# Kernel optimization log

Measured on AMD Instinct MI355X. Metric: run time of the kernel, lower is better.

The kernel has to match this reference:

```python
import jax, jax.numpy as jnp
import numpy as np

N = 100000      # nodes
E = 1600000     # edges (avg degree 16)
EL = 200000     # supervision (label) edges
D_IN, D_HID, D_OUT = 128, 128, 64


def setup_inputs() -> dict:
    key = jax.random.key(0)
    k = jax.random.split(key, 6)
    x = jax.random.normal(k[0], (N, D_IN), jnp.float32)
    edge_index = jax.random.randint(k[1], (2, E), 0, N, dtype=jnp.int32)
    edge_label_index = jax.random.randint(k[2], (2, EL), 0, N, dtype=jnp.int32)
    W1 = jax.random.normal(k[3], (D_IN, D_HID), jnp.float32) * (1.0 / np.sqrt(D_IN))
    b1 = jnp.zeros((D_HID,), jnp.float32)
    W2 = jax.random.normal(k[4], (D_HID, D_OUT), jnp.float32) * (1.0 / np.sqrt(D_HID))
    b2 = jnp.zeros((D_OUT,), jnp.float32)
    return {"x": x, "edge_index": edge_index, "edge_label_index": edge_label_index,
            "W1": W1, "b1": b1, "W2": W2, "b2": b2}


def gcn_layer(x, src, dst, W, b, n):
    """PyG-style GCNConv: linear -> sym-normalized scatter-add with self loops -> +bias."""
    h = x @ W                                   # [N, F]
    ones = jnp.ones(src.shape[0], h.dtype)
    deg = jax.ops.segment_sum(ones, dst, num_segments=n) + 1.0   # in-degree + self loop
    dinv = jax.lax.rsqrt(deg)                   # deg^{-1/2}
    norm = dinv[src] * dinv[dst]                # per-edge norm
    agg = jax.ops.segment_sum(h[src] * norm[:, None], dst, num_segments=n)
    agg = agg + h * (1.0 / deg)[:, None]        # self-loop contribution: dinv[i]^2
    return agg + b


def reference(x, edge_index, edge_label_index, W1, b1, W2, b2):
    src, dst = edge_index[0], edge_index[1]
    z = gcn_layer(x, src, dst, W1, b1, N)
    z = jax.nn.relu(z)                          # dropout omitted (eval mode)
    z = gcn_layer(z, src, dst, W2, b2, N)
    # decode: gather-dot over supervision edges
    return (z[edge_label_index[0]] * z[edge_label_index[1]]).sum(axis=-1)
```

## Files before the change

### kernel.cpp

```cpp
#include <hip/hip_runtime.h>
#include <stdint.h>

typedef __bf16 bf16x8 __attribute__((ext_vector_type(8)));
typedef float  floatx4 __attribute__((ext_vector_type(4)));
typedef __fp16 h2 __attribute__((ext_vector_type(2)));

__device__ __forceinline__ unsigned short f2b(float x){
    unsigned u = __float_as_uint(x);
    u = u + 0x7FFFu + ((u >> 16) & 1u);
    return (unsigned short)(u >> 16);
}
__device__ __forceinline__ float b2f(unsigned short h){
    return __uint_as_float(((unsigned)h) << 16);
}


__global__ __launch_bounds__(256) void k_scatter2(const int* __restrict__ src,
                                                  const int* __restrict__ dst,
                                                  int* __restrict__ gcur,
                                                  unsigned* __restrict__ slab,
                                                  int E_, int nbins){
    __shared__ int h[1024];
    int t = threadIdx.x, blk = blockIdx.x;
    for (int i = t; i < nbins; i += 256) h[i] = 0;
    __syncthreads();
    int base = blk * 8192;
    #pragma unroll
    for (int j = 0; j < 8; j++){
        int e = base + (j * 256 + t) * 4;
        if (e < E_){
            int4 d = *(const int4*)(dst + e);
            atomicAdd(&h[d.x >> 7], 1);
            atomicAdd(&h[d.y >> 7], 1);
            atomicAdd(&h[d.z >> 7], 1);
            atomicAdd(&h[d.w >> 7], 1);
        }
    }
    __syncthreads();
    for (int i = t; i < nbins; i += 256){
        int hv = h[i];
        h[i] = hv ? atomicAdd(&gcur[i], hv) : 0;
    }
    __syncthreads();
    #pragma unroll
    for (int j = 0; j < 8; j++){
        int e = base + (j * 256 + t) * 4;
        if (e < E_){
            int4 d = *(const int4*)(dst + e);
            int4 s = *(const int4*)(src + e);
            int p0 = atomicAdd(&h[d.x >> 7], 1);
            slab[(size_t)(d.x >> 7) * 4096 + p0] = ((unsigned)(d.x & 127) << 25) | (unsigned)s.x;
            int p1 = atomicAdd(&h[d.y >> 7], 1);
            slab[(size_t)(d.y >> 7) * 4096 + p1] = ((unsigned)(d.y & 127) << 25) | (unsigned)s.y;
            int p2 = atomicAdd(&h[d.z >> 7], 1);
            slab[(size_t)(d.z >> 7) * 4096 + p2] = ((unsigned)(d.z & 127) << 25) | (unsigned)s.z;
            int p3 = atomicAdd(&h[d.w >> 7], 1);
            slab[(size_t)(d.w >> 7) * 4096 + p3] = ((unsigned)(d.w & 127) << 25) | (unsigned)s.w;
        }
    }
}

__global__ __launch_bounds__(1024) void k_binscanB(const int* __restrict__ btot,
                                                   int* __restrict__ boff, int nbins){
    __shared__ int s[1024];
    int t = threadIdx.x;
    s[t] = (t < nbins) ? btot[t] : 0;
    __syncthreads();
    for (int o = 1; o < 1024; o <<= 1){
        int v = (t >= o) ? s[t - o] : 0;
        __syncthreads();
        s[t] += v;
        __syncthreads();
    }
    if (t == 0) boff[0] = 0;
    if (t < nbins) boff[t + 1] = s[t];
}

__global__ __launch_bounds__(256) void k_binsort(const unsigned* __restrict__ slab,
                                                 const int* __restrict__ boff,
                                                 int* __restrict__ csr,
                                                 int* __restrict__ cnt,
                                                 int* __restrict__ off,
                                                 float* __restrict__ dinv,
                                                 int n, int nbins){
    int b = blockIdx.x, t = threadIdx.x;
    int s0 = boff[b], len = boff[b + 1] - s0;
    if (len > 4096) len = 4096;
    const unsigned* seg = slab + (size_t)b * 4096;
    __shared__ int cl[128], sc[128], cur[128];
    __shared__ unsigned buf[4096], outb[4096];
    if (t < 128){ cl[t] = 0; cur[t] = 0; }
    __syncthreads();
    for (int i = t; i < len; i += 256) buf[i] = seg[i];
    __syncthreads();
    for (int i = t; i < len; i += 256) atomicAdd(&cl[buf[i] >> 25], 1);
    __syncthreads();
    if (t < 128) sc[t] = cl[t];
    __syncthreads();
    for (int o = 1; o < 128; o <<= 1){
        int v = 0;
        if (t < 128 && t >= o) v = sc[t - o];
        __syncthreads();
        if (t < 128) sc[t] += v;
        __syncthreads();
    }
    for (int i = t; i < len; i += 256){
        unsigned w = buf[i];
        int nd = (int)(w >> 25);
        int p = (sc[nd] - cl[nd]) + atomicAdd(&cur[nd], 1);
        outb[p] = w & 0x1FFFFFFu;
    }
    __syncthreads();
    for (int i = t; i < len; i += 256) csr[s0 + i] = (int)outb[i];
    if (t < 128){
        int node = b * 128 + t;
        if (node < n){
            cnt[node] = cl[t];
            off[node] = s0 + (sc[t] - cl[t]);
            dinv[node] = rsqrtf((float)cl[t] + 1.0f);
        }
    }
}

__global__ __launch_bounds__(256) void k_wconv(const float* __restrict__ W1,
                                               const float* __restrict__ W2,
                                               unsigned short* __restrict__ wf1,
                                               unsigned* __restrict__ w2p){
    int f = blockIdx.x * 256 + threadIdx.x;
    if (f < 2048){
        int lane = f & 63;
        int ctkc = f >> 6;
        int kc = ctkc & 3, ct = ctkc >> 2;
        int col = ct * 16 + (lane & 15);
        int k0  = kc * 32 + (lane >> 4) * 8;
        unsigned short* d = wf1 + (size_t)f * 8;
        #pragma unroll
        for (int j = 0; j < 8; j++) d[j] = f2b(W1[(k0 + j) * 128 + col]);
    } else if (f < 2048 + 4096){
        int lf = f - 2048;
        int kp = lf >> 6, lane = lf & 63;
        h2 p = __builtin_amdgcn_cvt_pkrtz(W2[(2 * kp) * 64 + lane],
                                          W2[(2 * kp + 1) * 64 + lane]);
        w2p[lf] = __builtin_bit_cast(unsigned, p);
    }
}

__global__ __launch_bounds__(256) void k_gemm1(const float* __restrict__ x,
                                               const unsigned short* __restrict__ wf,
                                               const float* __restrict__ dinv,
                                               unsigned short* __restrict__ hs, int n){
    __shared__ unsigned short Wl[16384];
    __shared__ unsigned short Al[64 * 136];
    int t = threadIdx.x;
    long rowBase = (long)blockIdx.x * 64;
    {
        const uint4* s4 = (const uint4*)wf;
        uint4* d4 = (uint4*)Wl;
        #pragma unroll
        for (int i = 0; i < 8; i++) d4[t + i * 256] = s4[t + i * 256];
    }
    {
        const float4* xs = (const float4*)(x + rowBase * 128);
        #pragma unroll
        for (int k = 0; k < 8; k++){
            int i = t + k * 256;
            int r = i >> 5, c4 = (i & 31) << 2;
            float4 v = make_float4(0.f, 0.f, 0.f, 0.f);
            if (rowBase + r < n) v = xs[i];
            unsigned lo = (unsigned)f2b(v.x) | ((unsigned)f2b(v.y) << 16);
            unsigned hi = (unsigned)f2b(v.z) | ((unsigned)f2b(v.w) << 16);
            *(uint2*)&Al[r * 136 + c4] = make_uint2(lo, hi);
        }
    }
    __syncthreads();
    int w = t >> 6, lane = t & 63, lr = lane & 15, q = lane >> 4;
    floatx4 zero = {0.f, 0.f, 0.f, 0.f};
    floatx4 acc[8];
    #pragma unroll
    for (int ct = 0; ct < 8; ct++) acc[ct] = zero;
    #pragma unroll
    for (int kc = 0; kc < 4; kc++){
        bf16x8 af = *(const bf16x8*)&Al[(w * 16 + lr) * 136 + kc * 32 + q * 8];
        #pragma unroll
        for (int ct = 0; ct < 8; ct++){
            bf16x8 bf = *(const bf16x8*)&Wl[((ct * 4 + kc) * 64 + lane) * 8];
            acc[ct] = __builtin_amdgcn_mfma_f32_16x16x32_bf16(af, bf, acc[ct], 0, 0, 0);
        }
    }
    long r0 = rowBase + w * 16 + q * 4;
    #pragma unroll
    for (int r = 0; r < 4; r++){
        long row = r0 + r;
        if (row >= n) continue;
        float dv = dinv[row];
        unsigned short* orow = hs + row * 128 + lr;
        #pragma unroll
        for (int ct = 0; ct < 8; ct++) orow[ct * 16] = f2b(acc[ct][r] * dv);
    }
}

__global__ __launch_bounds__(256) void k_agg1g2(const unsigned short* __restrict__ hs,
                                                const int* __restrict__ off,
                                                const int* __restrict__ cnt,
                                                const int* __restrict__ csr,
                                                const float* __restrict__ dinv,
                                                const float* __restrict__ b1,
                                                const unsigned* __restrict__ w2p,
                                                unsigned short* __restrict__ hs2,
                                                int n, int nwaves){
    __shared__ unsigned W2l[4096];
    __shared__ unsigned zp[4][64];
    int t = threadIdx.x;
    {
        const uint4* w4 = (const uint4*)w2p;
        uint4* d4 = (uint4*)W2l;
        #pragma unroll
        for (int i = 0; i < 4; i++) d4[t + i * 256] = w4[t + i * 256];
    }
    __syncthreads();
    int wband = t >> 6, lane = t & 63;
    float2 bb = ((const float2*)b1)[lane];
    for (int wid = blockIdx.x * 4 + wband; wid < n; wid += nwaves){
        size_t i = (size_t)wid;
        int start = off[wid], c = cnt[wid];
        unsigned v0 = *(const unsigned*)(hs + i * 128 + lane * 2);
        float a0 = b2f((unsigned short)v0);
        float a1 = b2f((unsigned short)(v0 >> 16));
        int j = 0;
        for (; j + 8 <= c; j += 8){
            size_t s0 = (size_t)csr[start + j + 0];
            size_t s1 = (size_t)csr[start + j + 1];
            size_t s2 = (size_t)csr[start + j + 2];
            size_t s3 = (size_t)csr[start + j + 3];
            size_t s4 = (size_t)csr[start + j + 4];
            size_t s5 = (size_t)csr[start + j + 5];
            size_t s6 = (size_t)csr[start + j + 6];
            size_t s7 = (size_t)csr[start + j + 7];
            unsigned w0 = *(const unsigned*)(hs + s0 * 128 + lane * 2);
            unsigned w1 = *(const unsigned*)(hs + s1 * 128 + lane * 2);
            unsigned w2 = *(const unsigned*)(hs + s2 * 128 + lane * 2);
            unsigned w3 = *(const unsigned*)(hs + s3 * 128 + lane * 2);
            unsigned w4 = *(const unsigned*)(hs + s4 * 128 + lane * 2);
            unsigned w5 = *(const unsigned*)(hs + s5 * 128 + lane * 2);
            unsigned w6 = *(const unsigned*)(hs + s6 * 128 + lane * 2);
            unsigned w7 = *(const unsigned*)(hs + s7 * 128 + lane * 2);
            a0 += b2f((unsigned short)w0); a1 += b2f((unsigned short)(w0 >> 16));
            a0 += b2f((unsigned short)w1); a1 += b2f((unsigned short)(w1 >> 16));
            a0 += b2f((unsigned short)w2); a1 += b2f((unsigned short)(w2 >> 16));
            a0 += b2f((unsigned short)w3); a1 += b2f((unsigned short)(w3 >> 16));
            a0 += b2f((unsigned short)w4); a1 += b2f((unsigned short)(w4 >> 16));
            a0 += b2f((unsigned short)w5); a1 += b2f((unsigned short)(w5 >> 16));
            a0 += b2f((unsigned short)w6); a1 += b2f((unsigned short)(w6 >> 16));
            a0 += b2f((unsigned short)w7); a1 += b2f((unsigned short)(w7 >> 16));
        }
        for (; j < c; j++){
            size_t s = (size_t)csr[start + j];
            unsigned v = *(const unsigned*)(hs + s * 128 + lane * 2);
            a0 += b2f((unsigned short)v);
            a1 += b2f((unsigned short)(v >> 16));
        }
        float dv = dinv[wid];
        float z0 = fmaxf(fmaf(dv, a0, bb.x), 0.f);
        float z1 = fmaxf(fmaf(dv, a1, bb.y), 0.f);
        zp[wband][lane] = __builtin_bit_cast(unsigned, __builtin_amdgcn_cvt_pkrtz(z0, z1));
        float acc0 = 0.f, acc1 = 0.f;
        #pragma unroll 8
        for (int kp = 0; kp < 64; kp += 2){
            h2 wa = __builtin_bit_cast(h2, W2l[kp * 64 + lane]);
            h2 wb = __builtin_bit_cast(h2, W2l[(kp + 1) * 64 + lane]);
            h2 za = __builtin_bit_cast(h2, zp[wband][kp]);
            h2 zb = __builtin_bit_cast(h2, zp[wband][kp + 1]);
            acc0 = __builtin_amdgcn_fdot2(za, wa, acc0, false);
            acc1 = __builtin_amdgcn_fdot2(zb, wb, acc1, false);
        }
        hs2[i * 64 + lane] = f2b((acc0 + acc1) * dv);
    }
}

__global__ __launch_bounds__(256) void k_agg2(const unsigned short* __restrict__ hs,
                                              const int* __restrict__ off,
                                              const int* __restrict__ cnt,
                                              const int* __restrict__ csr,
                                              const float* __restrict__ dinv,
                                              const float* __restrict__ b,
                                              unsigned short* __restrict__ z, int n){
    int wv = (blockIdx.x * 256 + threadIdx.x) >> 6;
    int lane = threadIdx.x & 63;
    int half = lane >> 5, hl = lane & 31;
    int node = wv * 2 + half;
    if (node >= n) return;
    size_t i = (size_t)node;
    int start = off[node], c = cnt[node];
    unsigned v0 = *(const unsigned*)(hs + i * 64 + hl * 2);
    float a0 = b2f((unsigned short)v0);
    float a1 = b2f((unsigned short)(v0 >> 16));
    int j = 0;
    for (; j + 8 <= c; j += 8){
        size_t s0 = (size_t)csr[start + j + 0];
        size_t s1 = (size_t)csr[start + j + 1];
        size_t s2 = (size_t)csr[start + j + 2];
        size_t s3 = (size_t)csr[start + j + 3];
        size_t s4 = (size_t)csr[start + j + 4];
        size_t s5 = (size_t)csr[start + j + 5];
        size_t s6 = (size_t)csr[start + j + 6];
        size_t s7 = (size_t)csr[start + j + 7];
        unsigned w0 = *(const unsigned*)(hs + s0 * 64 + hl * 2);
        unsigned w1 = *(const unsigned*)(hs + s1 * 64 + hl * 2);
        unsigned w2 = *(const unsigned*)(hs + s2 * 64 + hl * 2);
        unsigned w3 = *(const unsigned*)(hs + s3 * 64 + hl * 2);
        unsigned w4 = *(const unsigned*)(hs + s4 * 64 + hl * 2);
        unsigned w5 = *(const unsigned*)(hs + s5 * 64 + hl * 2);
        unsigned w6 = *(const unsigned*)(hs + s6 * 64 + hl * 2);
        unsigned w7 = *(const unsigned*)(hs + s7 * 64 + hl * 2);
        a0 += b2f((unsigned short)w0); a1 += b2f((unsigned short)(w0 >> 16));
        a0 += b2f((unsigned short)w1); a1 += b2f((unsigned short)(w1 >> 16));
        a0 += b2f((unsigned short)w2); a1 += b2f((unsigned short)(w2 >> 16));
        a0 += b2f((unsigned short)w3); a1 += b2f((unsigned short)(w3 >> 16));
        a0 += b2f((unsigned short)w4); a1 += b2f((unsigned short)(w4 >> 16));
        a0 += b2f((unsigned short)w5); a1 += b2f((unsigned short)(w5 >> 16));
        a0 += b2f((unsigned short)w6); a1 += b2f((unsigned short)(w6 >> 16));
        a0 += b2f((unsigned short)w7); a1 += b2f((unsigned short)(w7 >> 16));
    }
    for (; j < c; j++){
        size_t s = (size_t)csr[start + j];
        unsigned v = *(const unsigned*)(hs + s * 64 + hl * 2);
        a0 += b2f((unsigned short)v);
        a1 += b2f((unsigned short)(v >> 16));
    }
    float dv = dinv[node];
    float2 bb = ((const float2*)b)[hl];
    float r0 = fmaf(dv, a0, bb.x);
    float r1 = fmaf(dv, a1, bb.y);
    *(unsigned*)(z + i * 64 + hl * 2) = (unsigned)f2b(r0) | ((unsigned)f2b(r1) << 16);
}

__global__ __launch_bounds__(256) void k_decode(const unsigned short* __restrict__ z,
                                                const int* __restrict__ es,
                                                const int* __restrict__ et,
                                                float* __restrict__ out, int m){
    int wv = (blockIdx.x * 256 + threadIdx.x) >> 6;
    int lane = threadIdx.x & 63;
    int e = wv * 4 + (lane >> 4);
    int ql = lane & 15;
    float p = 0.f;
    if (e < m){
        size_t s = (size_t)es[e], t2 = (size_t)et[e];
        uint2 vs = *(const uint2*)(z + s * 64 + ql * 4);
        uint2 vt = *(const uint2*)(z + t2 * 64 + ql * 4);
        p = b2f((unsigned short)vs.x) * b2f((unsigned short)vt.x)
          + b2f((unsigned short)(vs.x >> 16)) * b2f((unsigned short)(vt.x >> 16))
          + b2f((unsigned short)vs.y) * b2f((unsigned short)vt.y)
          + b2f((unsigned short)(vs.y >> 16)) * b2f((unsigned short)(vt.y >> 16));
    }
    #pragma unroll
    for (int o = 8; o > 0; o >>= 1) p += __shfl_xor(p, o);
    if (ql == 0 && e < m) out[e] = p;
}


extern "C" void kernel_launch(void* const* d_in, const int* in_sizes, int n_in,
                              void* d_out, int out_size, void* d_ws, size_t ws_size,
                              hipStream_t stream){
    const float* x   = (const float*)d_in[0];
    const int*   ei  = (const int*)d_in[1];
    const int*   eli = (const int*)d_in[2];
    const float* W1  = (const float*)d_in[3];
    const float* b1  = (const float*)d_in[4];
    const float* W2  = (const float*)d_in[5];
    const float* b2  = (const float*)d_in[6];
    float* out = (float*)d_out;

    int N_  = in_sizes[0] / 128;
    int E_  = in_sizes[1] / 2;
    int EL_ = in_sizes[2] / 2;
    int NBINS = (N_ + 127) >> 7;
    const int EPB = 8192;
    int NBLK = (E_ + EPB - 1) / EPB;

    char* w = (char*)d_ws;
    size_t o = 0;
    auto alloc = [&](size_t bytes) -> size_t {
        size_t r = o; o += (bytes + 511) & ~(size_t)511; return r;
    };
    size_t o_cnt  = alloc((size_t)N_ * 4);
    size_t o_off  = alloc((size_t)N_ * 4);
    size_t o_dinv = alloc((size_t)N_ * 4);
    size_t o_gcur = alloc((size_t)NBINS * 4);
    size_t o_boff = alloc((size_t)(NBINS + 1) * 4);
    size_t o_csr  = alloc((size_t)E_ * 4);
    size_t o_wf1  = alloc(16384 * 2);
    size_t o_w2p  = alloc(4096 * 4);
    size_t o_hs1  = alloc((size_t)N_ * 128 * 2);
    size_t o_hs2  = alloc((size_t)N_ * 64 * 2);

    int* cnt  = (int*)(w + o_cnt);
    int* off  = (int*)(w + o_off);
    float* dinv = (float*)(w + o_dinv);
    int* gcur = (int*)(w + o_gcur);
    int* boff = (int*)(w + o_boff);
    int* csr  = (int*)(w + o_csr);
    unsigned short* wf1 = (unsigned short*)(w + o_wf1);
    unsigned* w2p = (unsigned*)(w + o_w2p);
    unsigned short* hs1 = (unsigned short*)(w + o_hs1);
    unsigned short* hs2 = (unsigned short*)(w + o_hs2);
    unsigned short* z2  = (unsigned short*)(w + o_hs1);

    unsigned* slab = (unsigned*)(w + o_hs1);

    const int AGG1_BLOCKS = 2048;
    int nwaves = AGG1_BLOCKS * 4;

    (void)hipMemsetAsync(gcur, 0, (size_t)NBINS * 4, stream);
    k_scatter2<<<NBLK, 256, 0, stream>>>(ei, ei + E_, gcur, slab, E_, NBINS);
    k_binscanB<<<1, 1024, 0, stream>>>(gcur, boff, NBINS);
    k_binsort <<<NBINS, 256, 0, stream>>>(slab, boff, csr, cnt, off, dinv, N_, NBINS);
    k_wconv   <<<24, 256, 0, stream>>>(W1, W2, wf1, w2p);
    k_gemm1   <<<(N_ + 63) / 64, 256, 0, stream>>>(x, wf1, dinv, hs1, N_);
    k_agg1g2  <<<AGG1_BLOCKS, 256, 0, stream>>>(hs1, off, cnt, csr, dinv, b1, w2p, hs2, N_, nwaves);
    k_agg2    <<<(N_ + 7) / 8, 256, 0, stream>>>(hs2, off, cnt, csr, dinv, b2, z2, N_);
    k_decode  <<<(EL_ + 15) / 16, 256, 0, stream>>>(z2, eli, eli + EL_, out, EL_);
}
```

Before: 279.5 us.

## Use column-sliced feature layout for gathers and split layer-2 GEMM into MFMA kernel

Node feature tables are now stored as 16-column slices (slice-major), and the aggregation kernels assign one slice per block, so each gather reads a 32-byte row piece from a slice table of about 3.2 MB. That slice table fits in cache far better than the full 256-byte-row table, which cuts DRAM traffic on random neighbor reads. The fused agg1 plus fdot2 layer-2 GEMM is split into a separate aggregation and an MFMA bf16 GEMM kernel, and the CSR index loads become nontemporal. In exchange, the edge index list is re-read once per slice (8 times for layer 1, 4 for layer 2), and z1 makes an extra round trip through memory.

```diff
diff --git a/kernel.cpp b/kernel.cpp
--- a/kernel.cpp
+++ b/kernel.cpp
@@ -3,7 +3,6 @@
 
 typedef __bf16 bf16x8 __attribute__((ext_vector_type(8)));
 typedef float  floatx4 __attribute__((ext_vector_type(4)));
-typedef __fp16 h2 __attribute__((ext_vector_type(2)));
 
 __device__ __forceinline__ unsigned short f2b(float x){
     unsigned u = __float_as_uint(x);
@@ -125,24 +124,20 @@
 __global__ __launch_bounds__(256) void k_wconv(const float* __restrict__ W1,
                                                const float* __restrict__ W2,
                                                unsigned short* __restrict__ wf1,
-                                               unsigned* __restrict__ w2p){
+                                               unsigned short* __restrict__ wf2){
     int f = blockIdx.x * 256 + threadIdx.x;
-    if (f < 2048){
-        int lane = f & 63;
-        int ctkc = f >> 6;
-        int kc = ctkc & 3, ct = ctkc >> 2;
-        int col = ct * 16 + (lane & 15);
-        int k0  = kc * 32 + (lane >> 4) * 8;
-        unsigned short* d = wf1 + (size_t)f * 8;
-        #pragma unroll
-        for (int j = 0; j < 8; j++) d[j] = f2b(W1[(k0 + j) * 128 + col]);
-    } else if (f < 2048 + 4096){
-        int lf = f - 2048;
-        int kp = lf >> 6, lane = lf & 63;
-        h2 p = __builtin_amdgcn_cvt_pkrtz(W2[(2 * kp) * 64 + lane],
-                                          W2[(2 * kp + 1) * 64 + lane]);
-        w2p[lf] = __builtin_bit_cast(unsigned, p);
-    }
+    if (f >= 3072) return;
+    const float* W; unsigned short* o; int ncol, lf;
+    if (f < 2048){ W = W1; o = wf1; ncol = 128; lf = f; }
+    else         { W = W2; o = wf2; ncol = 64;  lf = f - 2048; }
+    int lane = lf & 63;
+    int ctkc = lf >> 6;
+    int kc = ctkc & 3, ct = ctkc >> 2;
+    int col = ct * 16 + (lane & 15);
+    int k0  = kc * 32 + (lane >> 4) * 8;
+    unsigned short* d = o + (size_t)lf * 8;
+    #pragma unroll
+    for (int j = 0; j < 8; j++) d[j] = f2b(W[(k0 + j) * ncol + col]);
 }
 
 __global__ __launch_bounds__(256) void k_gemm1(const float* __restrict__ x,
@@ -193,57 +188,55 @@
         long row = r0 + r;
         if (row >= n) continue;
         float dv = dinv[row];
-        unsigned short* orow = hs + row * 128 + lr;
-        #pragma unroll
-        for (int ct = 0; ct < 8; ct++) orow[ct * 16] = f2b(acc[ct][r] * dv);
-    }
-}
-
-__global__ __launch_bounds__(256) void k_agg1g2(const unsigned short* __restrict__ hs,
-                                                const int* __restrict__ off,
-                                                const int* __restrict__ cnt,
-                                                const int* __restrict__ csr,
-                                                const float* __restrict__ dinv,
-                                                const float* __restrict__ b1,
-                                                const unsigned* __restrict__ w2p,
-                                                unsigned short* __restrict__ hs2,
-                                                int n, int nwaves){
-    __shared__ unsigned W2l[4096];
-    __shared__ unsigned zp[4][64];
+        #pragma unroll
+        for (int ct = 0; ct < 8; ct++)
+            hs[((size_t)ct * n + row) * 16 + lr] = f2b(acc[ct][r] * dv);
+    }
+}
+
+__global__ __launch_bounds__(256) void k_cagg1(const unsigned short* __restrict__ hs,
+                                               const int* __restrict__ off,
+                                               const int* __restrict__ cnt,
+                                               const int* __restrict__ csr,
+                                               const float* __restrict__ dinv,
+                                               const float* __restrict__ b1,
+                                               unsigned short* __restrict__ z1,
+                                               int n, int nblocks){
     int t = threadIdx.x;
-    {
-        const uint4* w4 = (const uint4*)w2p;
-        uint4* d4 = (uint4*)W2l;
-        #pragma unroll
-        for (int i = 0; i < 4; i++) d4[t + i * 256] = w4[t + i * 256];
-    }
-    __syncthreads();
+    int slice = blockIdx.x & 7;
+    int sblk = blockIdx.x >> 3;
+    int nsb = nblocks >> 3;
     int wband = t >> 6, lane = t & 63;
-    float2 bb = ((const float2*)b1)[lane];
-    for (int wid = blockIdx.x * 4 + wband; wid < n; wid += nwaves){
-        size_t i = (size_t)wid;
-        int start = off[wid], c = cnt[wid];
-        unsigned v0 = *(const unsigned*)(hs + i * 128 + lane * 2);
+    int g = lane >> 3, sub = lane & 7;
+    const unsigned short* tab = hs + (size_t)slice * n * 16;
+    unsigned short* zt = z1 + (size_t)slice * n * 16;
+    float2 bb = *(const float2*)(b1 + slice * 16 + sub * 2);
+    int node0 = (sblk * 4 + wband) * 8 + g;
+    int stride = nsb * 4 * 8;
+    for (int node = node0; node < n; node += stride){
+        int start = off[node], c = cnt[node];
+        float dv = dinv[node];
+        unsigned v0 = *(const unsigned*)(tab + (size_t)node * 16 + sub * 2);
         float a0 = b2f((unsigned short)v0);
         float a1 = b2f((unsigned short)(v0 >> 16));
         int j = 0;
         for (; j + 8 <= c; j += 8){
-            size_t s0 = (size_t)csr[start + j + 0];
-            size_t s1 = (size_t)csr[start + j + 1];
-            size_t s2 = (size_t)csr[start + j + 2];
-            size_t s3 = (size_t)csr[start + j + 3];
-            size_t s4 = (size_t)csr[start + j + 4];
-            size_t s5 = (size_t)csr[start + j + 5];
-            size_t s6 = (size_t)csr[start + j + 6];
-            size_t s7 = (size_t)csr[start + j + 7];
-            unsigned w0 = *(const unsigned*)(hs + s0 * 128 + lane * 2);
-            unsigned w1 = *(const unsigned*)(hs + s1 * 128 + lane * 2);
-            unsigned w2 = *(const unsigned*)(hs + s2 * 128 + lane * 2);
-            unsigned w3 = *(const unsigned*)(hs + s3 * 128 + lane * 2);
-            unsigned w4 = *(const unsigned*)(hs + s4 * 128 + lane * 2);
-            unsigned w5 = *(const unsigned*)(hs + s5 * 128 + lane * 2);
-            unsigned w6 = *(const unsigned*)(hs + s6 * 128 + lane * 2);
-            unsigned w7 = *(const unsigned*)(hs + s7 * 128 + lane * 2);
+            int i0 = __builtin_nontemporal_load(csr + start + j + 0);
+            int i1 = __builtin_nontemporal_load(csr + start + j + 1);
+            int i2 = __builtin_nontemporal_load(csr + start + j + 2);
+            int i3 = __builtin_nontemporal_load(csr + start + j + 3);
+            int i4 = __builtin_nontemporal_load(csr + start + j + 4);
+            int i5 = __builtin_nontemporal_load(csr + start + j + 5);
+            int i6 = __builtin_nontemporal_load(csr + start + j + 6);
+            int i7 = __builtin_nontemporal_load(csr + start + j + 7);
+            unsigned w0 = *(const unsigned*)(tab + (size_t)i0 * 16 + sub * 2);
+            unsigned w1 = *(const unsigned*)(tab + (size_t)i1 * 16 + sub * 2);
+            unsigned w2 = *(const unsigned*)(tab + (size_t)i2 * 16 + sub * 2);
+            unsigned w3 = *(const unsigned*)(tab + (size_t)i3 * 16 + sub * 2);
+            unsigned w4 = *(const unsigned*)(tab + (size_t)i4 * 16 + sub * 2);
+            unsigned w5 = *(const unsigned*)(tab + (size_t)i5 * 16 + sub * 2);
+            unsigned w6 = *(const unsigned*)(tab + (size_t)i6 * 16 + sub * 2);
+            unsigned w7 = *(const unsigned*)(tab + (size_t)i7 * 16 + sub * 2);
             a0 += b2f((unsigned short)w0); a1 += b2f((unsigned short)(w0 >> 16));
             a0 += b2f((unsigned short)w1); a1 += b2f((unsigned short)(w1 >> 16));
             a0 += b2f((unsigned short)w2); a1 += b2f((unsigned short)(w2 >> 16));
@@ -254,84 +247,133 @@
             a0 += b2f((unsigned short)w7); a1 += b2f((unsigned short)(w7 >> 16));
         }
         for (; j < c; j++){
-            size_t s = (size_t)csr[start + j];
-            unsigned v = *(const unsigned*)(hs + s * 128 + lane * 2);
+            int s = __builtin_nontemporal_load(csr + start + j);
+            unsigned v = *(const unsigned*)(tab + (size_t)s * 16 + sub * 2);
             a0 += b2f((unsigned short)v);
             a1 += b2f((unsigned short)(v >> 16));
         }
-        float dv = dinv[wid];
         float z0 = fmaxf(fmaf(dv, a0, bb.x), 0.f);
-        float z1 = fmaxf(fmaf(dv, a1, bb.y), 0.f);
-        zp[wband][lane] = __builtin_bit_cast(unsigned, __builtin_amdgcn_cvt_pkrtz(z0, z1));
-        float acc0 = 0.f, acc1 = 0.f;
-        #pragma unroll 8
-        for (int kp = 0; kp < 64; kp += 2){
-            h2 wa = __builtin_bit_cast(h2, W2l[kp * 64 + lane]);
-            h2 wb = __builtin_bit_cast(h2, W2l[(kp + 1) * 64 + lane]);
-            h2 za = __builtin_bit_cast(h2, zp[wband][kp]);
-            h2 zb = __builtin_bit_cast(h2, zp[wband][kp + 1]);
-            acc0 = __builtin_amdgcn_fdot2(za, wa, acc0, false);
-            acc1 = __builtin_amdgcn_fdot2(zb, wb, acc1, false);
-        }
-        hs2[i * 64 + lane] = f2b((acc0 + acc1) * dv);
-    }
-}
-
-__global__ __launch_bounds__(256) void k_agg2(const unsigned short* __restrict__ hs,
-                                              const int* __restrict__ off,
-                                              const int* __restrict__ cnt,
-                                              const int* __restrict__ csr,
-                                              const float* __restrict__ dinv,
-                                              const float* __restrict__ b,
-                                              unsigned short* __restrict__ z, int n){
-    int wv = (blockIdx.x * 256 + threadIdx.x) >> 6;
-    int lane = threadIdx.x & 63;
-    int half = lane >> 5, hl = lane & 31;
-    int node = wv * 2 + half;
-    if (node >= n) return;
-    size_t i = (size_t)node;
-    int start = off[node], c = cnt[node];
-    unsigned v0 = *(const unsigned*)(hs + i * 64 + hl * 2);
-    float a0 = b2f((unsigned short)v0);
-    float a1 = b2f((unsigned short)(v0 >> 16));
-    int j = 0;
-    for (; j + 8 <= c; j += 8){
-        size_t s0 = (size_t)csr[start + j + 0];
-        size_t s1 = (size_t)csr[start + j + 1];
-        size_t s2 = (size_t)csr[start + j + 2];
-        size_t s3 = (size_t)csr[start + j + 3];
-        size_t s4 = (size_t)csr[start + j + 4];
-        size_t s5 = (size_t)csr[start + j + 5];
-        size_t s6 = (size_t)csr[start + j + 6];
-        size_t s7 = (size_t)csr[start + j + 7];
-        unsigned w0 = *(const unsigned*)(hs + s0 * 64 + hl * 2);
-        unsigned w1 = *(const unsigned*)(hs + s1 * 64 + hl * 2);
-        unsigned w2 = *(const unsigned*)(hs + s2 * 64 + hl * 2);
-        unsigned w3 = *(const unsigned*)(hs + s3 * 64 + hl * 2);
-        unsigned w4 = *(const unsigned*)(hs + s4 * 64 + hl * 2);
-        unsigned w5 = *(const unsigned*)(hs + s5 * 64 + hl * 2);
-        unsigned w6 = *(const unsigned*)(hs + s6 * 64 + hl * 2);
-        unsigned w7 = *(const unsigned*)(hs + s7 * 64 + hl * 2);
-        a0 += b2f((unsigned short)w0); a1 += b2f((unsigned short)(w0 >> 16));
-        a0 += b2f((unsigned short)w1); a1 += b2f((unsigned short)(w1 >> 16));
-        a0 += b2f((unsigned short)w2); a1 += b2f((unsigned short)(w2 >> 16));
-        a0 += b2f((unsigned short)w3); a1 += b2f((unsigned short)(w3 >> 16));
-        a0 += b2f((unsigned short)w4); a1 += b2f((unsigned short)(w4 >> 16));
-        a0 += b2f((unsigned short)w5); a1 += b2f((unsigned short)(w5 >> 16));
-        a0 += b2f((unsigned short)w6); a1 += b2f((unsigned short)(w6 >> 16));
-        a0 += b2f((unsigned short)w7); a1 += b2f((unsigned short)(w7 >> 16));
-    }
-    for (; j < c; j++){
-        size_t s = (size_t)csr[start + j];
-        unsigned v = *(const unsigned*)(hs + s * 64 + hl * 2);
-        a0 += b2f((unsigned short)v);
-        a1 += b2f((unsigned short)(v >> 16));
-    }
-    float dv = dinv[node];
-    float2 bb = ((const float2*)b)[hl];
-    float r0 = fmaf(dv, a0, bb.x);
-    float r1 = fmaf(dv, a1, bb.y);
-    *(unsigned*)(z + i * 64 + hl * 2) = (unsigned)f2b(r0) | ((unsigned)f2b(r1) << 16);
+        float zv = fmaxf(fmaf(dv, a1, bb.y), 0.f);
+        *(unsigned*)(zt + (size_t)node * 16 + sub * 2) =
+            (unsigned)f2b(z0) | ((unsigned)f2b(zv) << 16);
+    }
+}
+
+__global__ __launch_bounds__(256) void k_gemm2(const unsigned short* __restrict__ z1,
+                                               const unsigned short* __restrict__ wf,
+                                               const float* __restrict__ dinv,
+                                               unsigned short* __restrict__ hs2, int n){
+    __shared__ unsigned short Wl[8192];
+    __shared__ unsigned short Al[64 * 136];
+    int t = threadIdx.x;
+    long rowBase = (long)blockIdx.x * 64;
+    {
+        const uint4* s4 = (const uint4*)wf;
+        uint4* d4 = (uint4*)Wl;
+        #pragma unroll
+        for (int i = 0; i < 4; i++) d4[t + i * 256] = s4[t + i * 256];
+    }
+    {
+        #pragma unroll
+        for (int k = 0; k < 4; k++){
+            int i = t + k * 256;
+            int s = i >> 7, r = (i >> 1) & 63, hh = i & 1;
+            uint4 v = make_uint4(0u, 0u, 0u, 0u);
+            long row = rowBase + r;
+            if (row < n)
+                v = *(const uint4*)(z1 + ((size_t)s * n + row) * 16 + hh * 8);
+            *(uint4*)&Al[r * 136 + s * 16 + hh * 8] = v;
+        }
+    }
+    __syncthreads();
+    int w = t >> 6, lane = t & 63, lr = lane & 15, q = lane >> 4;
+    floatx4 zero = {0.f, 0.f, 0.f, 0.f};
+    floatx4 acc[4];
+    #pragma unroll
+    for (int ct = 0; ct < 4; ct++) acc[ct] = zero;
+    #pragma unroll
+    for (int kc = 0; kc < 4; kc++){
+        bf16x8 af = *(const bf16x8*)&Al[(w * 16 + lr) * 136 + kc * 32 + q * 8];
+        #pragma unroll
+        for (int ct = 0; ct < 4; ct++){
+            bf16x8 bf = *(const bf16x8*)&Wl[((ct * 4 + kc) * 64 + lane) * 8];
+            acc[ct] = __builtin_amdgcn_mfma_f32_16x16x32_bf16(af, bf, acc[ct], 0, 0, 0);
+        }
+    }
+    long r0 = rowBase + w * 16 + q * 4;
+    #pragma unroll
+    for (int r = 0; r < 4; r++){
+        long row = r0 + r;
+        if (row >= n) continue;
+        float dv = dinv[row];
+        #pragma unroll
+        for (int ct = 0; ct < 4; ct++)
+            hs2[((size_t)ct * n + row) * 16 + lr] = f2b(acc[ct][r] * dv);
+    }
+}
+
+__global__ __launch_bounds__(256) void k_cagg2(const unsigned short* __restrict__ hs,
+                                               const int* __restrict__ off,
+                                               const int* __restrict__ cnt,
+                                               const int* __restrict__ csr,
+                                               const float* __restrict__ dinv,
+                                               const float* __restrict__ b2,
+                                               unsigned short* __restrict__ z2,
+                                               int n, int nblocks){
+    int t = threadIdx.x;
+    int slice = blockIdx.x & 3;
+    int sblk = blockIdx.x >> 2;
+    int nsb = nblocks >> 2;
+    int wband = t >> 6, lane = t & 63;
+    int g = lane >> 3, sub = lane & 7;
+    const unsigned short* tab = hs + (size_t)slice * n * 16;
+    float2 bb = *(const float2*)(b2 + slice * 16 + sub * 2);
+    int node0 = (sblk * 4 + wband) * 8 + g;
+    int stride = nsb * 4 * 8;
+    for (int node = node0; node < n; node += stride){
+        int start = off[node], c = cnt[node];
+        float dv = dinv[node];
+        unsigned v0 = *(const unsigned*)(tab + (size_t)node * 16 + sub * 2);
+        float a0 = b2f((unsigned short)v0);
+        float a1 = b2f((unsigned short)(v0 >> 16));
+        int j = 0;
+        for (; j + 8 <= c; j += 8){
+            int i0 = __builtin_nontemporal_load(csr + start + j + 0);
+            int i1 = __builtin_nontemporal_load(csr + start + j + 1);
+            int i2 = __builtin_nontemporal_load(csr + start + j + 2);
+            int i3 = __builtin_nontemporal_load(csr + start + j + 3);
+            int i4 = __builtin_nontemporal_load(csr + start + j + 4);
+            int i5 = __builtin_nontemporal_load(csr + start + j + 5);
+            int i6 = __builtin_nontemporal_load(csr + start + j + 6);
+            int i7 = __builtin_nontemporal_load(csr + start + j + 7);
+            unsigned w0 = *(const unsigned*)(tab + (size_t)i0 * 16 + sub * 2);
+            unsigned w1 = *(const unsigned*)(tab + (size_t)i1 * 16 + sub * 2);
+            unsigned w2 = *(const unsigned*)(tab + (size_t)i2 * 16 + sub * 2);
+            unsigned w3 = *(const unsigned*)(tab + (size_t)i3 * 16 + sub * 2);
+            unsigned w4 = *(const unsigned*)(tab + (size_t)i4 * 16 + sub * 2);
+            unsigned w5 = *(const unsigned*)(tab + (size_t)i5 * 16 + sub * 2);
+            unsigned w6 = *(const unsigned*)(tab + (size_t)i6 * 16 + sub * 2);
+            unsigned w7 = *(const unsigned*)(tab + (size_t)i7 * 16 + sub * 2);
+            a0 += b2f((unsigned short)w0); a1 += b2f((unsigned short)(w0 >> 16));
+            a0 += b2f((unsigned short)w1); a1 += b2f((unsigned short)(w1 >> 16));
+            a0 += b2f((unsigned short)w2); a1 += b2f((unsigned short)(w2 >> 16));
+            a0 += b2f((unsigned short)w3); a1 += b2f((unsigned short)(w3 >> 16));
+            a0 += b2f((unsigned short)w4); a1 += b2f((unsigned short)(w4 >> 16));
+            a0 += b2f((unsigned short)w5); a1 += b2f((unsigned short)(w5 >> 16));
+            a0 += b2f((unsigned short)w6); a1 += b2f((unsigned short)(w6 >> 16));
+            a0 += b2f((unsigned short)w7); a1 += b2f((unsigned short)(w7 >> 16));
+        }
+        for (; j < c; j++){
+            int s = __builtin_nontemporal_load(csr + start + j);
+            unsigned v = *(const unsigned*)(tab + (size_t)s * 16 + sub * 2);
+            a0 += b2f((unsigned short)v);
+            a1 += b2f((unsigned short)(v >> 16));
+        }
+        float r0 = fmaf(dv, a0, bb.x);
+        float r1 = fmaf(dv, a1, bb.y);
+        *(unsigned*)(z2 + (size_t)node * 64 + slice * 16 + sub * 2) =
+            (unsigned)f2b(r0) | ((unsigned)f2b(r1) << 16);
+    }
 }
 
 __global__ __launch_bounds__(256) void k_decode(const unsigned short* __restrict__ z,
@@ -389,9 +431,9 @@
     size_t o_boff = alloc((size_t)(NBINS + 1) * 4);
     size_t o_csr  = alloc((size_t)E_ * 4);
     size_t o_wf1  = alloc(16384 * 2);
-    size_t o_w2p  = alloc(4096 * 4);
+    size_t o_wf2  = alloc(8192 * 2);
     size_t o_hs1  = alloc((size_t)N_ * 128 * 2);
-    size_t o_hs2  = alloc((size_t)N_ * 64 * 2);
+    size_t o_z1   = alloc((size_t)N_ * 128 * 2);
 
     int* cnt  = (int*)(w + o_cnt);
     int* off  = (int*)(w + o_off);
@@ -400,23 +442,23 @@
     int* boff = (int*)(w + o_boff);
     int* csr  = (int*)(w + o_csr);
     unsigned short* wf1 = (unsigned short*)(w + o_wf1);
-    unsigned* w2p = (unsigned*)(w + o_w2p);
+    unsigned short* wf2 = (unsigned short*)(w + o_wf2);
     unsigned short* hs1 = (unsigned short*)(w + o_hs1);
-    unsigned short* hs2 = (unsigned short*)(w + o_hs2);
-    unsigned short* z2  = (unsigned short*)(w + o_hs1);
-
+    unsigned short* z1  = (unsigned short*)(w + o_z1);
+    unsigned short* hs2 = (unsigned short*)(w + o_hs1);
+    unsigned short* z2  = (unsigned short*)(w + o_hs1 + (size_t)N_ * 64 * 2);
     unsigned* slab = (unsigned*)(w + o_hs1);
 
-    const int AGG1_BLOCKS = 2048;
-    int nwaves = AGG1_BLOCKS * 4;
+    const int GBLK = 2048;
 
     (void)hipMemsetAsync(gcur, 0, (size_t)NBINS * 4, stream);
     k_scatter2<<<NBLK, 256, 0, stream>>>(ei, ei + E_, gcur, slab, E_, NBINS);
     k_binscanB<<<1, 1024, 0, stream>>>(gcur, boff, NBINS);
     k_binsort <<<NBINS, 256, 0, stream>>>(slab, boff, csr, cnt, off, dinv, N_, NBINS);
-    k_wconv   <<<24, 256, 0, stream>>>(W1, W2, wf1, w2p);
+    k_wconv   <<<12, 256, 0, stream>>>(W1, W2, wf1, wf2);
     k_gemm1   <<<(N_ + 63) / 64, 256, 0, stream>>>(x, wf1, dinv, hs1, N_);
-    k_agg1g2  <<<AGG1_BLOCKS, 256, 0, stream>>>(hs1, off, cnt, csr, dinv, b1, w2p, hs2, N_, nwaves);
-    k_agg2    <<<(N_ + 7) / 8, 256, 0, stream>>>(hs2, off, cnt, csr, dinv, b2, z2, N_);
+    k_cagg1   <<<GBLK, 256, 0, stream>>>(hs1, off, cnt, csr, dinv, b1, z1, N_, GBLK);
+    k_gemm2   <<<(N_ + 63) / 64, 256, 0, stream>>>(z1, wf2, dinv, hs2, N_);
+    k_cagg2   <<<GBLK, 256, 0, stream>>>(hs2, off, cnt, csr, dinv, b2, z2, N_, GBLK);
     k_decode  <<<(EL_ + 15) / 16, 256, 0, stream>>>(z2, eli, eli + EL_, out, EL_);
 }
```

After: 408.7 us. +46.2%, slower.

## Split neighbor gathers across wave sub-groups with wider loads and shuffle reduction

Applied to the files above, without the earlier changes.

In both aggregation kernels, each wave now processes several neighbors at once: layer 1 splits the wave into two halves, each loading 8 bytes per lane from a different neighbor row, and layer 2 gives one node per wave, split into four 16-lane groups. Partial sums are combined with xor shuffles before the self-loop term, bias and ReLU are applied. The aim is more memory-level parallelism per wave and wider loads for the random row gathers. The cost is extra shuffle work, more idle lanes on low-degree remainders, and twice as many waves launched for layer 2.

```diff
diff --git a/kernel.cpp b/kernel.cpp
--- a/kernel.cpp
+++ b/kernel.cpp
@@ -219,50 +219,75 @@
     }
     __syncthreads();
     int wband = t >> 6, lane = t & 63;
-    float2 bb = ((const float2*)b1)[lane];
+    int half = lane >> 5, hl = lane & 31;
+    float4 bb = ((const float4*)b1)[hl];
     for (int wid = blockIdx.x * 4 + wband; wid < n; wid += nwaves){
         size_t i = (size_t)wid;
         int start = off[wid], c = cnt[wid];
-        unsigned v0 = *(const unsigned*)(hs + i * 128 + lane * 2);
-        float a0 = b2f((unsigned short)v0);
-        float a1 = b2f((unsigned short)(v0 >> 16));
+        float a0 = 0.f, a1 = 0.f, a2 = 0.f, a3 = 0.f;
         int j = 0;
-        for (; j + 8 <= c; j += 8){
-            size_t s0 = (size_t)csr[start + j + 0];
-            size_t s1 = (size_t)csr[start + j + 1];
-            size_t s2 = (size_t)csr[start + j + 2];
-            size_t s3 = (size_t)csr[start + j + 3];
-            size_t s4 = (size_t)csr[start + j + 4];
-            size_t s5 = (size_t)csr[start + j + 5];
-            size_t s6 = (size_t)csr[start + j + 6];
-            size_t s7 = (size_t)csr[start + j + 7];
-            unsigned w0 = *(const unsigned*)(hs + s0 * 128 + lane * 2);
-            unsigned w1 = *(const unsigned*)(hs + s1 * 128 + lane * 2);
-            unsigned w2 = *(const unsigned*)(hs + s2 * 128 + lane * 2);
-            unsigned w3 = *(const unsigned*)(hs + s3 * 128 + lane * 2);
-            unsigned w4 = *(const unsigned*)(hs + s4 * 128 + lane * 2);
-            unsigned w5 = *(const unsigned*)(hs + s5 * 128 + lane * 2);
-            unsigned w6 = *(const unsigned*)(hs + s6 * 128 + lane * 2);
-            unsigned w7 = *(const unsigned*)(hs + s7 * 128 + lane * 2);
-            a0 += b2f((unsigned short)w0); a1 += b2f((unsigned short)(w0 >> 16));
-            a0 += b2f((unsigned short)w1); a1 += b2f((unsigned short)(w1 >> 16));
-            a0 += b2f((unsigned short)w2); a1 += b2f((unsigned short)(w2 >> 16));
-            a0 += b2f((unsigned short)w3); a1 += b2f((unsigned short)(w3 >> 16));
-            a0 += b2f((unsigned short)w4); a1 += b2f((unsigned short)(w4 >> 16));
-            a0 += b2f((unsigned short)w5); a1 += b2f((unsigned short)(w5 >> 16));
-            a0 += b2f((unsigned short)w6); a1 += b2f((unsigned short)(w6 >> 16));
-            a0 += b2f((unsigned short)w7); a1 += b2f((unsigned short)(w7 >> 16));
-        }
-        for (; j < c; j++){
-            size_t s = (size_t)csr[start + j];
-            unsigned v = *(const unsigned*)(hs + s * 128 + lane * 2);
-            a0 += b2f((unsigned short)v);
-            a1 += b2f((unsigned short)(v >> 16));
-        }
+        for (; j + 16 <= c; j += 16){
+            int i0 = csr[start + j +  0 + half];
+            int i1 = csr[start + j +  2 + half];
+            int i2 = csr[start + j +  4 + half];
+            int i3 = csr[start + j +  6 + half];
+            int i4 = csr[start + j +  8 + half];
+            int i5 = csr[start + j + 10 + half];
+            int i6 = csr[start + j + 12 + half];
+            int i7 = csr[start + j + 14 + half];
+            uint2 w0 = *(const uint2*)(hs + (size_t)i0 * 128 + hl * 4);
+            uint2 w1 = *(const uint2*)(hs + (size_t)i1 * 128 + hl * 4);
+            uint2 w2 = *(const uint2*)(hs + (size_t)i2 * 128 + hl * 4);
+            uint2 w3 = *(const uint2*)(hs + (size_t)i3 * 128 + hl * 4);
+            uint2 w4 = *(const uint2*)(hs + (size_t)i4 * 128 + hl * 4);
+            uint2 w5 = *(const uint2*)(hs + (size_t)i5 * 128 + hl * 4);
+            uint2 w6 = *(const uint2*)(hs + (size_t)i6 * 128 + hl * 4);
+            uint2 w7 = *(const uint2*)(hs + (size_t)i7 * 128 + hl * 4);
+            a0 += b2f((unsigned short)w0.x); a1 += b2f((unsigned short)(w0.x >> 16));
+            a2 += b2f((unsigned short)w0.y); a3 += b2f((unsigned short)(w0.y >> 16));
+            a0 += b2f((unsigned short)w1.x); a1 += b2f((unsigned short)(w1.x >> 16));
+            a2 += b2f((unsigned short)w1.y); a3 += b2f((unsigned short)(w1.y >> 16));
+            a0 += b2f((unsigned short)w2.x); a1 += b2f((unsigned short)(w2.x >> 16));
+            a2 += b2f((unsigned short)w2.y); a3 += b2f((unsigned short)(w2.y >> 16));
+            a0 += b2f((unsigned short)w3.x); a1 += b2f((unsigned short)(w3.x >> 16));
+            a2 += b2f((unsigned short)w3.y); a3 += b2f((unsigned short)(w3.y >> 16));
+            a0 += b2f((unsigned short)w4.x); a1 += b2f((unsigned short)(w4.x >> 16));
+            a2 += b2f((unsigned short)w4.y); a3 += b2f((unsigned short)(w4.y >> 16));
+            a0 += b2f((unsigned short)w5.x); a1 += b2f((unsigned short)(w5.x >> 16));
+            a2 += b2f((unsigned short)w5.y); a3 += b2f((unsigned short)(w5.y >> 16));
+            a0 += b2f((unsigned short)w6.x); a1 += b2f((unsigned short)(w6.x >> 16));
+            a2 += b2f((unsigned short)w6.y); a3 += b2f((unsigned short)(w6.y >> 16));
+            a0 += b2f((unsigned short)w7.x); a1 += b2f((unsigned short)(w7.x >> 16));
+            a2 += b2f((unsigned short)w7.y); a3 += b2f((unsigned short)(w7.y >> 16));
+        }
+        for (; j + 2 <= c; j += 2){
+            int s = csr[start + j + half];
+            uint2 v = *(const uint2*)(hs + (size_t)s * 128 + hl * 4);
+            a0 += b2f((unsigned short)v.x); a1 += b2f((unsigned short)(v.x >> 16));
+            a2 += b2f((unsigned short)v.y); a3 += b2f((unsigned short)(v.y >> 16));
+        }
+        if (j < c && half == 0){
+            int s = csr[start + j];
+            uint2 v = *(const uint2*)(hs + (size_t)s * 128 + hl * 4);
+            a0 += b2f((unsigned short)v.x); a1 += b2f((unsigned short)(v.x >> 16));
+            a2 += b2f((unsigned short)v.y); a3 += b2f((unsigned short)(v.y >> 16));
+        }
+        a0 += __shfl_xor(a0, 32);
+        a1 += __shfl_xor(a1, 32);
+        a2 += __shfl_xor(a2, 32);
+        a3 += __shfl_xor(a3, 32);
+        uint2 sv = *(const uint2*)(hs + i * 128 + hl * 4);
+        a0 += b2f((unsigned short)sv.x); a1 += b2f((unsigned short)(sv.x >> 16));
+        a2 += b2f((unsigned short)sv.y); a3 += b2f((unsigned short)(sv.y >> 16));
         float dv = dinv[wid];
         float z0 = fmaxf(fmaf(dv, a0, bb.x), 0.f);
         float z1 = fmaxf(fmaf(dv, a1, bb.y), 0.f);
-        zp[wband][lane] = __builtin_bit_cast(unsigned, __builtin_amdgcn_cvt_pkrtz(z0, z1));
+        float z2 = fmaxf(fmaf(dv, a2, bb.z), 0.f);
+        float z3 = fmaxf(fmaf(dv, a3, bb.w), 0.f);
+        if (half == 0){
+            zp[wband][2 * hl]     = __builtin_bit_cast(unsigned, __builtin_amdgcn_cvt_pkrtz(z0, z1));
+            zp[wband][2 * hl + 1] = __builtin_bit_cast(unsigned, __builtin_amdgcn_cvt_pkrtz(z2, z3));
+        }
         float acc0 = 0.f, acc1 = 0.f;
         #pragma unroll 8
         for (int kp = 0; kp < 64; kp += 2){
@@ -284,54 +309,59 @@
                                               const float* __restrict__ dinv,
                                               const float* __restrict__ b,
                                               unsigned short* __restrict__ z, int n){
-    int wv = (blockIdx.x * 256 + threadIdx.x) >> 6;
+    int node = (blockIdx.x * 256 + threadIdx.x) >> 6;
     int lane = threadIdx.x & 63;
-    int half = lane >> 5, hl = lane & 31;
-    int node = wv * 2 + half;
     if (node >= n) return;
+    int g = lane >> 4, q = lane & 15;
     size_t i = (size_t)node;
     int start = off[node], c = cnt[node];
-    unsigned v0 = *(const unsigned*)(hs + i * 64 + hl * 2);
-    float a0 = b2f((unsigned short)v0);
-    float a1 = b2f((unsigned short)(v0 >> 16));
+    float a0 = 0.f, a1 = 0.f, a2 = 0.f, a3 = 0.f;
     int j = 0;
-    for (; j + 8 <= c; j += 8){
-        size_t s0 = (size_t)csr[start + j + 0];
-        size_t s1 = (size_t)csr[start + j + 1];
-        size_t s2 = (size_t)csr[start + j + 2];
-        size_t s3 = (size_t)csr[start + j + 3];
-        size_t s4 = (size_t)csr[start + j + 4];
-        size_t s5 = (size_t)csr[start + j + 5];
-        size_t s6 = (size_t)csr[start + j + 6];
-        size_t s7 = (size_t)csr[start + j + 7];
-        unsigned w0 = *(const unsigned*)(hs + s0 * 64 + hl * 2);
-        unsigned w1 = *(const unsigned*)(hs + s1 * 64 + hl * 2);
-        unsigned w2 = *(const unsigned*)(hs + s2 * 64 + hl * 2);
-        unsigned w3 = *(const unsigned*)(hs + s3 * 64 + hl * 2);
-        unsigned w4 = *(const unsigned*)(hs + s4 * 64 + hl * 2);
-        unsigned w5 = *(const unsigned*)(hs + s5 * 64 + hl * 2);
-        unsigned w6 = *(const unsigned*)(hs + s6 * 64 + hl * 2);
-        unsigned w7 = *(const unsigned*)(hs + s7 * 64 + hl * 2);
-        a0 += b2f((unsigned short)w0); a1 += b2f((unsigned short)(w0 >> 16));
-        a0 += b2f((unsigned short)w1); a1 += b2f((unsigned short)(w1 >> 16));
-        a0 += b2f((unsigned short)w2); a1 += b2f((unsigned short)(w2 >> 16));
-        a0 += b2f((unsigned short)w3); a1 += b2f((unsigned short)(w3 >> 16));
-        a0 += b2f((unsigned short)w4); a1 += b2f((unsigned short)(w4 >> 16));
-        a0 += b2f((unsigned short)w5); a1 += b2f((unsigned short)(w5 >> 16));
-        a0 += b2f((unsigned short)w6); a1 += b2f((unsigned short)(w6 >> 16));
-        a0 += b2f((unsigned short)w7); a1 += b2f((unsigned short)(w7 >> 16));
-    }
-    for (; j < c; j++){
-        size_t s = (size_t)csr[start + j];
-        unsigned v = *(const unsigned*)(hs + s * 64 + hl * 2);
-        a0 += b2f((unsigned short)v);
-        a1 += b2f((unsigned short)(v >> 16));
-    }
+    for (; j + 16 <= c; j += 16){
+        int i0 = csr[start + j +  0 + g];
+        int i1 = csr[start + j +  4 + g];
+        int i2 = csr[start + j +  8 + g];
+        int i3 = csr[start + j + 12 + g];
+        uint2 w0 = *(const uint2*)(hs + (size_t)i0 * 64 + q * 4);
+        uint2 w1 = *(const uint2*)(hs + (size_t)i1 * 64 + q * 4);
+        uint2 w2 = *(const uint2*)(hs + (size_t)i2 * 64 + q * 4);
+        uint2 w3 = *(const uint2*)(hs + (size_t)i3 * 64 + q * 4);
+        a0 += b2f((unsigned short)w0.x); a1 += b2f((unsigned short)(w0.x >> 16));
+        a2 += b2f((unsigned short)w0.y); a3 += b2f((unsigned short)(w0.y >> 16));
+        a0 += b2f((unsigned short)w1.x); a1 += b2f((unsigned short)(w1.x >> 16));
+        a2 += b2f((unsigned short)w1.y); a3 += b2f((unsigned short)(w1.y >> 16));
+        a0 += b2f((unsigned short)w2.x); a1 += b2f((unsigned short)(w2.x >> 16));
+        a2 += b2f((unsigned short)w2.y); a3 += b2f((unsigned short)(w2.y >> 16));
+        a0 += b2f((unsigned short)w3.x); a1 += b2f((unsigned short)(w3.x >> 16));
+        a2 += b2f((unsigned short)w3.y); a3 += b2f((unsigned short)(w3.y >> 16));
+    }
+    for (; j + 4 <= c; j += 4){
+        int s = csr[start + j + g];
+        uint2 v = *(const uint2*)(hs + (size_t)s * 64 + q * 4);
+        a0 += b2f((unsigned short)v.x); a1 += b2f((unsigned short)(v.x >> 16));
+        a2 += b2f((unsigned short)v.y); a3 += b2f((unsigned short)(v.y >> 16));
+    }
+    int rem = c - j;
+    if (g < rem){
+        int s = csr[start + j + g];
+        uint2 v = *(const uint2*)(hs + (size_t)s * 64 + q * 4);
+        a0 += b2f((unsigned short)v.x); a1 += b2f((unsigned short)(v.x >> 16));
+        a2 += b2f((unsigned short)v.y); a3 += b2f((unsigned short)(v.y >> 16));
+    }
+    a0 += __shfl_xor(a0, 16); a1 += __shfl_xor(a1, 16);
+    a2 += __shfl_xor(a2, 16); a3 += __shfl_xor(a3, 16);
+    a0 += __shfl_xor(a0, 32); a1 += __shfl_xor(a1, 32);
+    a2 += __shfl_xor(a2, 32); a3 += __shfl_xor(a3, 32);
+    uint2 sv = *(const uint2*)(hs + i * 64 + q * 4);
+    a0 += b2f((unsigned short)sv.x); a1 += b2f((unsigned short)(sv.x >> 16));
+    a2 += b2f((unsigned short)sv.y); a3 += b2f((unsigned short)(sv.y >> 16));
     float dv = dinv[node];
-    float2 bb = ((const float2*)b)[hl];
-    float r0 = fmaf(dv, a0, bb.x);
-    float r1 = fmaf(dv, a1, bb.y);
-    *(unsigned*)(z + i * 64 + hl * 2) = (unsigned)f2b(r0) | ((unsigned)f2b(r1) << 16);
+    float4 bb = ((const float4*)b)[q];
+    if (g == 0){
+        unsigned lo = (unsigned)f2b(fmaf(dv, a0, bb.x)) | ((unsigned)f2b(fmaf(dv, a1, bb.y)) << 16);
+        unsigned hi = (unsigned)f2b(fmaf(dv, a2, bb.z)) | ((unsigned)f2b(fmaf(dv, a3, bb.w)) << 16);
+        *(uint2*)(z + i * 64 + q * 4) = make_uint2(lo, hi);
+    }
 }
 
 __global__ __launch_bounds__(256) void k_decode(const unsigned short* __restrict__ z,
@@ -417,6 +447,6 @@
     k_wconv   <<<24, 256, 0, stream>>>(W1, W2, wf1, w2p);
     k_gemm1   <<<(N_ + 63) / 64, 256, 0, stream>>>(x, wf1, dinv, hs1, N_);
     k_agg1g2  <<<AGG1_BLOCKS, 256, 0, stream>>>(hs1, off, cnt, csr, dinv, b1, w2p, hs2, N_, nwaves);
-    k_agg2    <<<(N_ + 7) / 8, 256, 0, stream>>>(hs2, off, cnt, csr, dinv, b2, z2, N_);
+    k_agg2    <<<(N_ + 3) / 4, 256, 0, stream>>>(hs2, off, cnt, csr, dinv, b2, z2, N_);
     k_decode  <<<(EL_ + 15) / 16, 256, 0, stream>>>(z2, eli, eli + EL_, out, EL_);
 }
```

Measured after the change: 283.4 us. About the same (+1.4%).

## Stage edges in LDS during scatter and fold bin scan into binsort

Applied to the files above, without the earlier changes.

The scatter kernel now caches packed edge words and bin ids in shared memory on its first pass, so the second pass reads them from LDS instead of reloading src/dst from global memory. Edges per block drop from 8192 to 4096 to fit those buffers. The single-block bin prefix scan kernel is removed, and every binsort block recomputes the scan over the bin totals itself. This saves a launch and a global round trip, at the cost of redundant scan work per block and more LDS per scatter block.

```diff
diff --git a/kernel.cpp b/kernel.cpp
--- a/kernel.cpp
+++ b/kernel.cpp
@@ -13,7 +13,6 @@
 __device__ __forceinline__ float b2f(unsigned short h){
     return __uint_as_float(((unsigned)h) << 16);
 }
-
 
 __global__ __launch_bounds__(256) void k_scatter2(const int* __restrict__ src,
                                                   const int* __restrict__ dst,
@@ -21,15 +20,28 @@
                                                   unsigned* __restrict__ slab,
                                                   int E_, int nbins){
     __shared__ int h[1024];
+    __shared__ unsigned wbuf[4096];
+    __shared__ unsigned short bbuf[4096];
     int t = threadIdx.x, blk = blockIdx.x;
     for (int i = t; i < nbins; i += 256) h[i] = 0;
     __syncthreads();
-    int base = blk * 8192;
-    #pragma unroll
-    for (int j = 0; j < 8; j++){
-        int e = base + (j * 256 + t) * 4;
+    int base = blk * 4096;
+    int valid = E_ - base; if (valid > 4096) valid = 4096;
+    #pragma unroll
+    for (int j = 0; j < 4; j++){
+        int li = (j * 256 + t) * 4;
+        int e = base + li;
         if (e < E_){
             int4 d = *(const int4*)(dst + e);
+            int4 s = *(const int4*)(src + e);
+            wbuf[li + 0] = ((unsigned)(d.x & 127) << 25) | (unsigned)s.x;
+            wbuf[li + 1] = ((unsigned)(d.y & 127) << 25) | (unsigned)s.y;
+            wbuf[li + 2] = ((unsigned)(d.z & 127) << 25) | (unsigned)s.z;
+            wbuf[li + 3] = ((unsigned)(d.w & 127) << 25) | (unsigned)s.w;
+            bbuf[li + 0] = (unsigned short)(d.x >> 7);
+            bbuf[li + 1] = (unsigned short)(d.y >> 7);
+            bbuf[li + 2] = (unsigned short)(d.z >> 7);
+            bbuf[li + 3] = (unsigned short)(d.w >> 7);
             atomicAdd(&h[d.x >> 7], 1);
             atomicAdd(&h[d.y >> 7], 1);
             atomicAdd(&h[d.z >> 7], 1);
@@ -42,49 +54,45 @@
         h[i] = hv ? atomicAdd(&gcur[i], hv) : 0;
     }
     __syncthreads();
-    #pragma unroll
-    for (int j = 0; j < 8; j++){
-        int e = base + (j * 256 + t) * 4;
-        if (e < E_){
-            int4 d = *(const int4*)(dst + e);
-            int4 s = *(const int4*)(src + e);
-            int p0 = atomicAdd(&h[d.x >> 7], 1);
-            slab[(size_t)(d.x >> 7) * 4096 + p0] = ((unsigned)(d.x & 127) << 25) | (unsigned)s.x;
-            int p1 = atomicAdd(&h[d.y >> 7], 1);
-            slab[(size_t)(d.y >> 7) * 4096 + p1] = ((unsigned)(d.y & 127) << 25) | (unsigned)s.y;
-            int p2 = atomicAdd(&h[d.z >> 7], 1);
-            slab[(size_t)(d.z >> 7) * 4096 + p2] = ((unsigned)(d.z & 127) << 25) | (unsigned)s.z;
-            int p3 = atomicAdd(&h[d.w >> 7], 1);
-            slab[(size_t)(d.w >> 7) * 4096 + p3] = ((unsigned)(d.w & 127) << 25) | (unsigned)s.w;
-        }
-    }
-}
-
-__global__ __launch_bounds__(1024) void k_binscanB(const int* __restrict__ btot,
-                                                   int* __restrict__ boff, int nbins){
-    __shared__ int s[1024];
-    int t = threadIdx.x;
-    s[t] = (t < nbins) ? btot[t] : 0;
-    __syncthreads();
-    for (int o = 1; o < 1024; o <<= 1){
-        int v = (t >= o) ? s[t - o] : 0;
-        __syncthreads();
-        s[t] += v;
-        __syncthreads();
-    }
-    if (t == 0) boff[0] = 0;
-    if (t < nbins) boff[t + 1] = s[t];
+    for (int i = t; i < valid; i += 256){
+        int bin = bbuf[i];
+        int p = atomicAdd(&h[bin], 1);
+        slab[(size_t)bin * 4096 + p] = wbuf[i];
+    }
 }
 
 __global__ __launch_bounds__(256) void k_binsort(const unsigned* __restrict__ slab,
-                                                 const int* __restrict__ boff,
+                                                 const int* __restrict__ gcur,
                                                  int* __restrict__ csr,
                                                  int* __restrict__ cnt,
                                                  int* __restrict__ off,
                                                  float* __restrict__ dinv,
                                                  int n, int nbins){
     int b = blockIdx.x, t = threadIdx.x;
-    int s0 = boff[b], len = boff[b + 1] - s0;
+    __shared__ int sv[1024], sp[256];
+    #pragma unroll
+    for (int k = 0; k < 4; k++){
+        int i = t * 4 + k;
+        sv[i] = (i < nbins) ? gcur[i] : 0;
+    }
+    __syncthreads();
+    int a0 = sv[t * 4], a1 = sv[t * 4 + 1], a2 = sv[t * 4 + 2], a3 = sv[t * 4 + 3];
+    sp[t] = a0 + a1 + a2 + a3;
+    __syncthreads();
+    for (int o = 1; o < 256; o <<= 1){
+        int v = (t >= o) ? sp[t - o] : 0;
+        __syncthreads();
+        sp[t] += v;
+        __syncthreads();
+    }
+    int basep = t ? sp[t - 1] : 0;
+    sv[t * 4]     = basep;
+    sv[t * 4 + 1] = basep + a0;
+    sv[t * 4 + 2] = basep + a0 + a1;
+    sv[t * 4 + 3] = basep + a0 + a1 + a2;
+    __syncthreads();
+    int s0 = sv[b];
+    int len = gcur[b];
     if (len > 4096) len = 4096;
     const unsigned* seg = slab + (size_t)b * 4096;
     __shared__ int cl[128], sc[128], cur[128];
@@ -374,7 +382,7 @@
     int E_  = in_sizes[1] / 2;
     int EL_ = in_sizes[2] / 2;
     int NBINS = (N_ + 127) >> 7;
-    const int EPB = 8192;
+    const int EPB = 4096;
     int NBLK = (E_ + EPB - 1) / EPB;
 
     char* w = (char*)d_ws;
@@ -386,7 +394,6 @@
     size_t o_off  = alloc((size_t)N_ * 4);
     size_t o_dinv = alloc((size_t)N_ * 4);
     size_t o_gcur = alloc((size_t)NBINS * 4);
-    size_t o_boff = alloc((size_t)(NBINS + 1) * 4);
     size_t o_csr  = alloc((size_t)E_ * 4);
     size_t o_wf1  = alloc(16384 * 2);
     size_t o_w2p  = alloc(4096 * 4);
@@ -397,7 +404,6 @@
     int* off  = (int*)(w + o_off);
     float* dinv = (float*)(w + o_dinv);
     int* gcur = (int*)(w + o_gcur);
-    int* boff = (int*)(w + o_boff);
     int* csr  = (int*)(w + o_csr);
     unsigned short* wf1 = (unsigned short*)(w + o_wf1);
     unsigned* w2p = (unsigned*)(w + o_w2p);
@@ -412,8 +418,7 @@
 
     (void)hipMemsetAsync(gcur, 0, (size_t)NBINS * 4, stream);
     k_scatter2<<<NBLK, 256, 0, stream>>>(ei, ei + E_, gcur, slab, E_, NBINS);
-    k_binscanB<<<1, 1024, 0, stream>>>(gcur, boff, NBINS);
-    k_binsort <<<NBINS, 256, 0, stream>>>(slab, boff, csr, cnt, off, dinv, N_, NBINS);
+    k_binsort <<<NBINS, 256, 0, stream>>>(slab, gcur, csr, cnt, off, dinv, N_, NBINS);
     k_wconv   <<<24, 256, 0, stream>>>(W1, W2, wf1, w2p);
     k_gemm1   <<<(N_ + 63) / 64, 256, 0, stream>>>(x, wf1, dinv, hs1, N_);
     k_agg1g2  <<<AGG1_BLOCKS, 256, 0, stream>>>(hs1, off, cnt, csr, dinv, b1, w2p, hs2, N_, nwaves);
```

Measured after the change: 279.8 us. Within noise of the previous version (+0.1%).
